# Performance work log

Hardware: AMD Instinct MI355X
Metric: run time of the kernel (lower is better)

The kernel has to match this reference:

```python
import jax, jax.numpy as jnp
import numpy as np
from jax import lax

B, C, H, W = 2, 64, 384, 384
WS = 8; NH = 4; HD = C // NH; S = WS * WS  # 64 tokens per window
EPS = 1e-5


def setup_inputs() -> dict:
    key = jax.random.key(0)
    ks = jax.random.split(key, 16)
    def n(k, shape, s=0.02):
        return jax.random.normal(k, shape, jnp.float32) * s
    return {
        "x": jax.random.normal(ks[0], (B, C, H, W), jnp.float32),
        "norm1_w": jnp.ones((C,), jnp.float32), "norm1_b": jnp.zeros((C,), jnp.float32),
        "qkv_w": n(ks[1], (3 * C, C)), "qkv_b": jnp.zeros((3 * C,), jnp.float32),
        "pos_bias": n(ks[2], (1, S, NH, NH), 0.01),  # faithful: bias over (tokens, heads, heads)
        "out_w": n(ks[3], (C, C)), "out_b": jnp.zeros((C,), jnp.float32),
        "convp_w": n(ks[4], (C, C)), "convp_b": jnp.zeros((C,), jnp.float32),
        "pw1_w": n(ks[5], (C, C, 1)), "pw1_b": jnp.zeros((C,), jnp.float32),
        "dw1_w": n(ks[6], (C, 1, 3)), "dw1_b": jnp.zeros((C,), jnp.float32),
        "tok_w": n(ks[7], (C, C)), "tok_b": jnp.zeros((C,), jnp.float32),
        "norm2_w": jnp.ones((C,), jnp.float32), "norm2_b": jnp.zeros((C,), jnp.float32),
        "leff_pw_w": n(ks[8], (C, C, 1, 1)),
        "leff_dw_w": n(ks[9], (C, 1, 3, 3)), "leff_dw_b": jnp.zeros((C,), jnp.float32),
        "fc1_w": n(ks[10], (4 * C, C)), "fc1_b": jnp.zeros((4 * C,), jnp.float32),
        "fc2_w": n(ks[11], (C, 4 * C)), "fc2_b": jnp.zeros((C,), jnp.float32),
    }


def _ln_c(x, w, b):
    # channel-wise LayerNorm (Restormer 'WithBias') on (B,C,H,W), biased variance
    mu = x.mean(axis=1, keepdims=True)
    var = ((x - mu) ** 2).mean(axis=1, keepdims=True)
    return (x - mu) / jnp.sqrt(var + EPS) * w[None, :, None, None] + b[None, :, None, None]


def _lin(x, w, b):
    return x @ w.T + b


def _win_part(x):
    # (B,C,H,W) -> (B*nw, S, C); H,W divisible by WS so pad is a no-op
    b = x.shape[0]
    x = x.reshape(b, C, H // WS, WS, W // WS, WS)
    return x.transpose(0, 2, 4, 3, 5, 1).reshape(-1, S, C)


def _win_merge(wins):
    b = wins.shape[0] // ((H // WS) * (W // WS))
    x = wins.reshape(b, H // WS, W // WS, WS, WS, C)
    return x.transpose(0, 5, 1, 3, 2, 4).reshape(b, C, H, W)


def _remsa(xw, qkv_w, qkv_b, pos_bias, out_w, out_b, convp_w, convp_b,
           pw1_w, pw1_b, dw1_w, dw1_b, tok_w, tok_b):
    bw = xw.shape[0]
    qkv = _lin(xw, qkv_w, qkv_b).reshape(bw, S, NH, 3 * HD)
    q, k, v = jnp.split(qkv, 3, axis=-1)  # each (bw, S, NH, HD)
    # Faithful to source: NO head transpose -> attention mixes across the heads axis
    scores = jnp.einsum('bshd,bsgd->bshg', q, k) * (HD ** -0.5) + pos_bias  # (bw,S,NH,NH)
    attn = jax.nn.softmax(scores, axis=-1)
    ao = jnp.einsum('bshg,bsgd->bshd', attn, v).reshape(bw, S, C)
    ao = _lin(ao, out_w, out_b)
    # convolutional branch
    xc = _lin(xw, convp_w, convp_b).transpose(0, 2, 1)  # (bw, C, S)
    xc = jnp.einsum('bcs,oc->bos', xc, pw1_w[:, :, 0]) + pw1_b[None, :, None]  # 1x1 conv1d
    xc = lax.conv_general_dilated(xc, dw1_w, (1,), 'SAME', feature_group_count=C,
                                  dimension_numbers=('NCH', 'OIH', 'NCH')) + dw1_b[None, :, None]
    xc = _lin(xc.transpose(0, 2, 1), tok_w, tok_b)
    return ao + xc


def _leff(x, pw_w, dw_w, dw_b, fc1_w, fc1_b, fc2_w, fc2_b):
    b = x.shape[0]
    y = lax.conv_general_dilated(x, pw_w, (1, 1), 'SAME',
                                 dimension_numbers=('NCHW', 'OIHW', 'NCHW'))  # 1x1, no bias
    y = lax.conv_general_dilated(y, dw_w, (1, 1), 'SAME', feature_group_count=C,
                                 dimension_numbers=('NCHW', 'OIHW', 'NCHW')) + dw_b[None, :, None, None]
    y = y.transpose(0, 2, 3, 1).reshape(b, H * W, C)
    y = jax.nn.gelu(_lin(y, fc1_w, fc1_b), approximate=False)
    y = _lin(y, fc2_w, fc2_b)
    return y.reshape(b, H, W, C).transpose(0, 3, 1, 2)


def reference(x, norm1_w, norm1_b, qkv_w, qkv_b, pos_bias, out_w, out_b,
              convp_w, convp_b, pw1_w, pw1_b, dw1_w, dw1_b, tok_w, tok_b,
              norm2_w, norm2_b, leff_pw_w, leff_dw_w, leff_dw_b,
              fc1_w, fc1_b, fc2_w, fc2_b):
    xw = _win_part(_ln_c(x, norm1_w, norm1_b))
    r = _win_merge(_remsa(xw, qkv_w, qkv_b, pos_bias, out_w, out_b, convp_w, convp_b,
                          pw1_w, pw1_b, dw1_w, dw1_b, tok_w, tok_b))
    x = x + r
    x = x + _leff(_ln_c(x, norm2_w, norm2_b), leff_pw_w, leff_dw_w, leff_dw_b,
                  fc1_w, fc1_b, fc2_w, fc2_b)
    return x
```

## Files before the change

### kernel.cpp

```cpp
#include <hip/hip_runtime.h>
#include <hip/hip_bf16.h>
#include <math.h>

#define Bn 2
#define Cc 64
#define Hh 384
#define Ww 384
#define HW (Hh*Ww)
#define Tt (Bn*HW)

using f32x4  = __attribute__((ext_vector_type(4))) float;
using bf16x8 = __attribute__((ext_vector_type(8))) short;


__device__ __forceinline__ unsigned short f2bf_u(float f) {
  return __builtin_bit_cast(unsigned short, __float2bfloat16(f));
}
__device__ __forceinline__ float bf2f(unsigned short u) {
  union { unsigned u; float f; } v; v.u = ((unsigned)u) << 16;
  return v.f;
}
__device__ __forceinline__ float gelu_exact(float v) {
  return 0.5f * v * (1.0f + erff(v * 0.70710678118654752f));
}

__device__ __forceinline__ void stage_wtile(char* dst, const float* __restrict__ g, int rs, int tid) {
#pragma unroll
  for (int half = 0; half < 2; ++half) {
    int q = tid + half * 256;
    int row = q >> 3, ks = q & 7;
    const float* gp = g + (long)row * rs + ks * 8;
    float4 a = *(const float4*)gp;
    float4 b = *(const float4*)(gp + 4);
    bf16x8 o;
    o[0] = (short)f2bf_u(a.x); o[1] = (short)f2bf_u(a.y);
    o[2] = (short)f2bf_u(a.z); o[3] = (short)f2bf_u(a.w);
    o[4] = (short)f2bf_u(b.x); o[5] = (short)f2bf_u(b.y);
    o[6] = (short)f2bf_u(b.z); o[7] = (short)f2bf_u(b.w);
    *(bf16x8*)(dst + row * 128 + ((ks * 16) ^ ((row & 7) << 4))) = o;
  }
}

__device__ __forceinline__ void mfma64(const char* sA, const char* sB, int wid, int lane, f32x4 acc[4]) {
  const int r = lane & 15, kq = lane >> 4;
#pragma unroll
  for (int kh = 0; kh < 2; ++kh) {
    const int arow = wid * 16 + r;
    bf16x8 af = *(const bf16x8*)(sA + arow * 128 + ((kh * 64 + kq * 16) ^ ((arow & 7) << 4)));
#pragma unroll
    for (int nt = 0; nt < 4; ++nt) {
      const int brow = nt * 16 + r;
      bf16x8 bfv = *(const bf16x8*)(sB + brow * 128 + ((kh * 64 + kq * 16) ^ ((brow & 7) << 4)));
      acc[nt] = __builtin_amdgcn_mfma_f32_16x16x32_bf16(af, bfv, acc[nt], 0, 0, 0);
    }
  }
}


__global__ __launch_bounds__(512, 4) void kA(
    const float* __restrict__ x, unsigned short* __restrict__ x1g, unsigned short* __restrict__ yg,
    const float* __restrict__ n1w, const float* __restrict__ n1b,
    const float* __restrict__ qkvw, const float* __restrict__ qkvb,
    const float* __restrict__ posb,
    const float* __restrict__ outw, const float* __restrict__ outb,
    const float* __restrict__ cpw, const float* __restrict__ cpb,
    const float* __restrict__ pw1w, const float* __restrict__ pw1b,
    const float* __restrict__ dw1w, const float* __restrict__ dw1b,
    const float* __restrict__ tokw, const float* __restrict__ tokb,
    const float* __restrict__ n2w, const float* __restrict__ n2b,
    const float* __restrict__ lpw) {
  __shared__ char sX[16384];
  __shared__ char sW0[8192];
  __shared__ char sW1[8192];
  __shared__ char sQ[49152];

  const int tid = threadIdx.x;
  const int lane = tid & 63, wid = tid >> 6;
  const int fr = lane & 15, kq = lane >> 4;
  const int rtok = wid * 16 + fr;
  const int c0own = kq * 16;
  const int iy = wid, ix = fr;
  const int blk = blockIdx.x;
  const int b = blk / 1152;
  const int rr = blk - b * 1152;
  const int wy = rr / 24, wxp = rr - (rr / 24) * 24;
  const int h0 = wy * 8, w0 = wxp * 16;
  const long ibase = (long)b * HW;

  float4 wr0, wr1;
  const int wrow = tid >> 3, wc0 = (tid & 7) * 8;
  auto WLOAD = [&](const float* g) {
    const float* p = g + (long)wrow * 64 + wc0;
    wr0 = *(const float4*)p; wr1 = *(const float4*)(p + 4);
  };
  auto WSTORE = [&](char* dst) {
    bf16x8 o;
    o[0]=(short)f2bf_u(wr0.x); o[1]=(short)f2bf_u(wr0.y); o[2]=(short)f2bf_u(wr0.z); o[3]=(short)f2bf_u(wr0.w);
    o[4]=(short)f2bf_u(wr1.x); o[5]=(short)f2bf_u(wr1.y); o[6]=(short)f2bf_u(wr1.z); o[7]=(short)f2bf_u(wr1.w);
    *(bf16x8*)(dst + wrow * 128 + ((2 * wc0) ^ ((wrow & 7) << 4))) = o;
  };

  WLOAD(cpw);
  const float* xb = x + ((long)(b * 64 + c0own)) * HW + (long)(h0 + iy) * Ww + (w0 + ix);
  float vx[16]; float s0 = 0.f, s1 = 0.f;
#pragma unroll
  for (int k = 0; k < 16; ++k) {
    float v = xb[(long)k * HW];
    vx[k] = v; s0 += v; s1 += v * v;
  }
  s0 += __shfl_xor(s0, 16); s0 += __shfl_xor(s0, 32);
  s1 += __shfl_xor(s1, 16); s1 += __shfl_xor(s1, 32);
  {
    float m = s0 * (1.f / 64.f);
    float ri = rsqrtf(s1 * (1.f / 64.f) - m * m + 1e-5f);
    const int swz = (rtok & 7) << 4;
#pragma unroll
    for (int q8 = 0; q8 < 2; ++q8) {
      bf16x8 o;
#pragma unroll
      for (int j = 0; j < 8; ++j) {
        int c = c0own + q8 * 8 + j;
        o[j] = (short)f2bf_u((vx[q8 * 8 + j] - m) * ri * n1w[c] + n1b[c]);
      }
      *(bf16x8*)(sX + rtok * 128 + ((c0own * 2 + q8 * 16) ^ swz)) = o;
    }
  }
  WSTORE(sW0); WLOAD(pw1w);
  __syncthreads();

  f32x4 acc[4], res[4];
  auto ZERO = [&](f32x4 a[4]) {
#pragma unroll
    for (int nt = 0; nt < 4; ++nt) a[nt] = (f32x4){0.f, 0.f, 0.f, 0.f};
  };
  auto GEMM = [&](const char* A, const char* W, f32x4 a[4]) {
#pragma unroll
    for (int kh = 0; kh < 2; ++kh) {
      const int arow = wid * 16 + fr;
      bf16x8 af = *(const bf16x8*)(A + arow * 128 + ((kh * 64 + kq * 16) ^ ((arow & 7) << 4)));
#pragma unroll
      for (int nt = 0; nt < 4; ++nt) {
        const int brow = nt * 16 + fr;
        bf16x8 bv = *(const bf16x8*)(W + brow * 128 + ((kh * 64 + kq * 16) ^ ((brow & 7) << 4)));
        a[nt] = __builtin_amdgcn_mfma_f32_16x16x32_bf16(af, bv, a[nt], 0, 0, 0);
      }
    }
  };
  auto EPI = [&](char* dst, f32x4 a[4], const float* bias) {
    const int rb = wid * 16 + kq * 4;
#pragma unroll
    for (int nt = 0; nt < 4; ++nt) {
      const int col = nt * 16 + fr;
      const float bv = bias[col];
#pragma unroll
      for (int reg = 0; reg < 4; ++reg) {
        const int row = rb + reg;
        *(unsigned short*)(dst + row * 128 + ((2 * col) ^ ((row & 7) << 4))) = f2bf_u(a[nt][reg] + bv);
      }
    }
  };
  char* t0 = sQ; char* t1 = sQ + 16384; char* t2 = sQ + 32768;
  float* sQf = (float*)sQ;

  ZERO(acc); GEMM(sX, sW0, acc); EPI(t0, acc, cpb);
  WSTORE(sW1); WLOAD(tokw);
  __syncthreads();
  ZERO(acc); GEMM(t0, sW1, acc); EPI(t1, acc, pw1b);
  WSTORE(sW0); WLOAD(qkvw);
  __syncthreads();
  {
    const int c = tid & 63, tq = tid >> 6;
    const int wl = tq >> 2, chunk = tq & 3;
    float wv0 = dw1w[c * 3], wv1 = dw1w[c * 3 + 1], wv2 = dw1w[c * 3 + 2], bia = dw1b[c];
#pragma unroll
    for (int k = 0; k < 16; ++k) {
      int s = chunk * 16 + k;
      int r0 = ((s >> 3) << 4) + wl * 8 + (s & 7);
      float v = bia + bf2f(*(const unsigned short*)(t1 + r0 * 128 + ((2 * c) ^ ((r0 & 7) << 4)))) * wv1;
      if (s > 0) {
        int rm = (((s - 1) >> 3) << 4) + wl * 8 + ((s - 1) & 7);
        v += bf2f(*(const unsigned short*)(t1 + rm * 128 + ((2 * c) ^ ((rm & 7) << 4)))) * wv0;
      }
      if (s < 63) {
        int rp = (((s + 1) >> 3) << 4) + wl * 8 + ((s + 1) & 7);
        v += bf2f(*(const unsigned short*)(t1 + rp * 128 + ((2 * c) ^ ((rp & 7) << 4)))) * wv2;
      }
      *(unsigned short*)(t0 + r0 * 128 + ((2 * c) ^ ((r0 & 7) << 4))) = f2bf_u(v);
    }
  }
  WSTORE(sW1); WLOAD(qkvw + 4096);
  __syncthreads();
  ZERO(res); GEMM(t0, sW0, res);
  __syncthreads();
  ZERO(acc); GEMM(sX, sW1, acc); EPI(t0, acc, qkvb);
  WSTORE(sW0); WLOAD(qkvw + 8192);
  __syncthreads();
  ZERO(acc); GEMM(sX, sW0, acc); EPI(t1, acc, qkvb + 64);
  WSTORE(sW1); WLOAD(outw);
  __syncthreads();
  ZERO(acc); GEMM(sX, sW1, acc); EPI(t2, acc, qkvb + 128);
  WSTORE(sW0); WLOAD(lpw);
  __syncthreads();
  {
    const int r = rtok;
    const int h = kq;
    const int s = ((r >> 4) << 3) + (r & 7);
    const int swz = (r & 7) << 4;
    auto LD16 = [&](int gcol, float* o) {
      const char* base = sQ + ((gcol >> 6) * 16384) + r * 128;
      int c0 = (gcol & 63) * 2;
      bf16x8 u = *(const bf16x8*)(base + (c0 ^ swz));
      bf16x8 w2_ = *(const bf16x8*)(base + ((c0 + 16) ^ swz));
#pragma unroll
      for (int j = 0; j < 8; ++j) {
        o[j] = bf2f((unsigned short)u[j]); o[8 + j] = bf2f((unsigned short)w2_[j]);
      }
    };
    float q0[16];
    LD16(48 * h, q0);
    float sc[4];
#pragma unroll
    for (int g = 0; g < 4; ++g) {
      float kk[16]; LD16(48 * g + 16, kk);
      float a = 0.f;
#pragma unroll
      for (int d = 0; d < 16; ++d) a += q0[d] * kk[d];
      sc[g] = a * 0.25f + posb[s * 16 + h * 4 + g];
    }
    float m = fmaxf(fmaxf(sc[0], sc[1]), fmaxf(sc[2], sc[3]));
    float e[4]; float tsum = 0.f;
#pragma unroll
    for (int g = 0; g < 4; ++g) { e[g] = __expf(sc[g] - m); tsum += e[g]; }
    float inv = 1.f / tsum;
    float ao[16];
#pragma unroll
    for (int d = 0; d < 16; ++d) ao[d] = 0.f;
#pragma unroll
    for (int g = 0; g < 4; ++g) {
      float vv[16]; LD16(48 * g + 32, vv);
#pragma unroll
      for (int d = 0; d < 16; ++d) ao[d] += e[g] * vv[d];
    }
    bf16x8 o1, o2;
#pragma unroll
    for (int j = 0; j < 8; ++j) { o1[j] = (short)f2bf_u(ao[j] * inv); o2[j] = (short)f2bf_u(ao[8 + j] * inv); }
    *(bf16x8*)(sX + r * 128 + ((h * 32) ^ swz)) = o1;
    *(bf16x8*)(sX + r * 128 + ((h * 32 + 16) ^ swz)) = o2;
  }
  WSTORE(sW1);
  __syncthreads();
  GEMM(sX, sW0, res);
  {
    const int rb = wid * 16 + kq * 4;
#pragma unroll
    for (int nt = 0; nt < 4; ++nt) {
      const int col = nt * 16 + fr;
      const float ob = outb[col] + tokb[col];
#pragma unroll
      for (int reg = 0; reg < 4; ++reg)
        sQf[(rb + reg) * 67 + col] = res[nt][reg] + ob;
    }
  }
  __syncthreads();
  {
    float ss0 = 0.f, ss1 = 0.f;
#pragma unroll
    for (int k = 0; k < 16; ++k) {
      float v = sQf[rtok * 67 + c0own + k] + vx[k];
      vx[k] = v; ss0 += v; ss1 += v * v;
    }
    ss0 += __shfl_xor(ss0, 16); ss0 += __shfl_xor(ss0, 32);
    ss1 += __shfl_xor(ss1, 16); ss1 += __shfl_xor(ss1, 32);
    float m = ss0 * (1.f / 64.f);
    float ri = rsqrtf(ss1 * (1.f / 64.f) - m * m + 1e-5f);
    const int swz = (rtok & 7) << 4;
    long t = ibase + (long)(h0 + iy) * Ww + (w0 + ix);
#pragma unroll
    for (int q8 = 0; q8 < 2; ++q8) {
      bf16x8 xo, no;
#pragma unroll
      for (int j = 0; j < 8; ++j) {
        int c = c0own + q8 * 8 + j;
        float v = vx[q8 * 8 + j];
        xo[j] = (short)f2bf_u(v);
        no[j] = (short)f2bf_u((v - m) * ri * n2w[c] + n2b[c]);
      }
      *(bf16x8*)((char*)x1g + t * 128 + (c0own + q8 * 8) * 2) = xo;
      *(bf16x8*)(sX + rtok * 128 + ((c0own * 2 + q8 * 16) ^ swz)) = no;
    }
  }
  __syncthreads();
  ZERO(acc); GEMM(sX, sW1, acc);
  {
    const int rb = wid * 16 + kq * 4;
#pragma unroll
    for (int nt = 0; nt < 4; ++nt) {
      const int col = nt * 16 + fr;
#pragma unroll
      for (int reg = 0; reg < 4; ++reg)
        sQf[(rb + reg) * 67 + col] = acc[nt][reg];
    }
  }
  __syncthreads();
  {
    long t = ibase + (long)(h0 + iy) * Ww + (w0 + ix);
#pragma unroll
    for (int q8 = 0; q8 < 2; ++q8) {
      bf16x8 o;
#pragma unroll
      for (int j = 0; j < 8; ++j)
        o[j] = (short)f2bf_u(sQf[rtok * 67 + c0own + q8 * 8 + j]);
      *(bf16x8*)((char*)yg + t * 128 + (c0own + q8 * 8) * 2) = o;
    }
  }
}


__global__ __launch_bounds__(256, 3) void kB(
    const unsigned short* __restrict__ yg, const unsigned short* __restrict__ x1g,
    float* __restrict__ out,
    const float* __restrict__ ldw, const float* __restrict__ ldb,
    const float* __restrict__ f1w, const float* __restrict__ f1b,
    const float* __restrict__ f2w, const float* __restrict__ f2b) {
  __shared__ char sZ0[8192];
  __shared__ char sZ1[8192];
  __shared__ char U[33792];
  __shared__ float wtab[640];

  const int tid = threadIdx.x;
  const int lane = tid & 63, wid = tid >> 6;
  const int bid = blockIdx.x;
  const int b = bid / 1152;
  const int r2 = bid - b * 1152;
  const int hp = r2 / 6, wseg = r2 - (r2 / 6) * 6;
  const int h0 = hp * 2, w0 = wseg * 64;
  const long ibase = (long)b * HW;
  const int cbase = lane & 15;
  const int rbase = wid * 16 + (lane >> 4) * 4;

  unsigned short x1r[2][4][4];
#pragma unroll
  for (int t = 0; t < 2; ++t) {
    const long p0t = ibase + (long)(h0 + t) * Ww + w0;
#pragma unroll
    for (int nt = 0; nt < 4; ++nt) {
      int col = nt * 16 + cbase;
#pragma unroll
      for (int reg = 0; reg < 4; ++reg)
        x1r[t][nt][reg] = x1g[(p0t + rbase + reg) * 64 + col];
    }
  }

#pragma unroll
  for (int it = 0; it < 3; ++it) {
    int idx = it * 256 + tid;
    if (idx < 576) wtab[idx] = ldw[(idx & 63) * 9 + (idx >> 6)];
    else if (idx < 640) wtab[idx] = ldb[idx - 576];
  }

  for (int it = 0; it < 9; ++it) {
    int idx = it * 256 + tid;
    if (idx >= 2112) break;
    int hr = idx / 528;
    int rq = idx - hr * 528;
    int px = rq >> 3, c8 = rq & 7;
    int h = h0 - 1 + hr, w = w0 - 1 + px;
    uint4 v = make_uint4(0, 0, 0, 0);
    if (h >= 0 && h < Hh && w >= 0 && w < Ww) {
      long t = ibase + (long)h * Ww + w;
      v = *(const uint4*)((const char*)yg + t * 128 + c8 * 16);
    }
    *(uint4*)(U + (hr * 66 + px) * 128 + c8 * 16) = v;
  }
  __syncthreads();

  {
    const int c8 = tid & 7, c0 = c8 * 8;
#pragma unroll
    for (int it = 0; it < 4; ++it) {
      int task = it * 256 + tid;
      int r = task >> 9;
      int px = (task >> 3) & 63;
      float a8[8];
#pragma unroll
      for (int j = 0; j < 8; ++j) a8[j] = wtab[576 + c0 + j];
#pragma unroll
      for (int dy = 0; dy < 3; ++dy)
#pragma unroll
        for (int dx = 0; dx < 3; ++dx) {
          bf16x8 v = *(const bf16x8*)(U + ((r + dy) * 66 + px + dx) * 128 + c8 * 16);
          const float* wk = wtab + (dy * 3 + dx) * 64 + c0;
#pragma unroll
          for (int j = 0; j < 8; ++j) a8[j] += bf2f((unsigned short)v[j]) * wk[j];
        }
      char* sZ = r ? sZ1 : sZ0;
      bf16x8 o;
#pragma unroll
      for (int j = 0; j < 8; ++j) o[j] = (short)f2bf_u(a8[j]);
      *(bf16x8*)(sZ + px * 128 + ((c8 * 16) ^ ((px & 7) << 4))) = o;
    }
  }
  __syncthreads();

  char* sW  = U;
  char* sH0 = U + 8192;
  char* sH1 = U + 16384;
  f32x4 res0[4], res1[4];
#pragma unroll
  for (int nt = 0; nt < 4; ++nt) { res0[nt] = (f32x4){0.f,0.f,0.f,0.f}; res1[nt] = (f32x4){0.f,0.f,0.f,0.f}; }

  for (int jc = 0; jc < 4; ++jc) {
    stage_wtile(sW, f1w + jc * 4096, 64, tid);
    __syncthreads();
#pragma unroll
    for (int t = 0; t < 2; ++t) {
      f32x4 acc[4];
#pragma unroll
      for (int nt = 0; nt < 4; ++nt) acc[nt] = (f32x4){0.f,0.f,0.f,0.f};
      mfma64(t ? sZ1 : sZ0, sW, wid, lane, acc);
      char* sH = t ? sH1 : sH0;
#pragma unroll
      for (int nt = 0; nt < 4; ++nt) {
        const int col = nt * 16 + cbase;
        const float bv = f1b[jc * 64 + col];
#pragma unroll
        for (int reg = 0; reg < 4; ++reg) {
          const int row = rbase + reg;
          *(unsigned short*)(sH + row * 128 + ((col * 2) ^ ((row & 7) << 4))) =
              f2bf_u(gelu_exact(acc[nt][reg] + bv));
        }
      }
    }
    __syncthreads();
    stage_wtile(sW, f2w + jc * 64, 256, tid);
    __syncthreads();
    mfma64(sH0, sW, wid, lane, res0);
    mfma64(sH1, sW, wid, lane, res1);
    __syncthreads();
  }

  float* sO = (float*)U;
#pragma unroll
  for (int t = 0; t < 2; ++t) {
    const f32x4* res = t ? res1 : res0;
#pragma unroll
    for (int nt = 0; nt < 4; ++nt) {
      const int col = nt * 16 + cbase;
      const float bv = f2b[col];
#pragma unroll
      for (int reg = 0; reg < 4; ++reg) {
        const int row = rbase + reg;
        sO[row * 65 + col] = res[nt][reg] + bv + bf2f(x1r[t][nt][reg]);
      }
    }
    __syncthreads();
#pragma unroll
    for (int it = 0; it < 16; ++it) {
      int c = it * 4 + (tid >> 6);
      int wo = tid & 63;
      out[(((long)(b * Cc + c)) * Hh + (h0 + t)) * Ww + w0 + wo] = sO[wo * 65 + c];
    }
    __syncthreads();
  }
}


extern "C" void kernel_launch(void* const* d_in, const int* in_sizes, int n_in,
                              void* d_out, int out_size, void* d_ws, size_t ws_size,
                              hipStream_t stream) {
  const float* x    = (const float*)d_in[0];
  const float* n1w  = (const float*)d_in[1];
  const float* n1b  = (const float*)d_in[2];
  const float* qkvw = (const float*)d_in[3];
  const float* qkvb = (const float*)d_in[4];
  const float* posb = (const float*)d_in[5];
  const float* outw = (const float*)d_in[6];
  const float* outb = (const float*)d_in[7];
  const float* cpw  = (const float*)d_in[8];
  const float* cpb  = (const float*)d_in[9];
  const float* pw1w = (const float*)d_in[10];
  const float* pw1b = (const float*)d_in[11];
  const float* dw1w = (const float*)d_in[12];
  const float* dw1b = (const float*)d_in[13];
  const float* tokw = (const float*)d_in[14];
  const float* tokb = (const float*)d_in[15];
  const float* n2w  = (const float*)d_in[16];
  const float* n2b  = (const float*)d_in[17];
  const float* lpw  = (const float*)d_in[18];
  const float* ldw  = (const float*)d_in[19];
  const float* ldb  = (const float*)d_in[20];
  const float* f1w  = (const float*)d_in[21];
  const float* f1b  = (const float*)d_in[22];
  const float* f2w  = (const float*)d_in[23];
  const float* f2b  = (const float*)d_in[24];
  float* out = (float*)d_out;

  unsigned short* x1 = (unsigned short*)d_ws;
  unsigned short* y  = x1 + (size_t)Tt * 64;

  kA<<<dim3(2304), dim3(512), 0, stream>>>(x, x1, y, n1w, n1b, qkvw, qkvb, posb,
                                           outw, outb, cpw, cpb, pw1w, pw1b,
                                           dw1w, dw1b, tokw, tokb, n2w, n2b, lpw);
  kB<<<dim3(2304), dim3(256), 0, stream>>>(y, x1, out, ldw, ldb, f1w, f1b, f2w, f2b);
}
```

Measured before the change: 184.7 us.

## Keep depthwise conv output in MFMA A-fragments in registers instead of LDS

The depthwise 3x3 conv in kB is remapped so each lane computes exactly the bf16 values it needs as MFMA A-operands for fc1, and keeps them in registers rather than writing them to the sZ0/sZ1 shared buffers. This removes 16KB of LDS per block and a round trip through shared memory, and launch bounds are raised from 3 to 4 blocks per CU. The staged input tile in U is XOR-swizzled to avoid bank conflicts under the new access pattern. The tighter launch bound adds register pressure, since the fragments stay live across the fc1/fc2 loop, and that may cause spills.

```diff
diff --git a/kernel.cpp b/kernel.cpp
--- a/kernel.cpp
+++ b/kernel.cpp
@@ -316,27 +316,26 @@
 }
 
 
-__global__ __launch_bounds__(256, 3) void kB(
+__global__ __launch_bounds__(256, 4) void kB(
     const unsigned short* __restrict__ yg, const unsigned short* __restrict__ x1g,
     float* __restrict__ out,
     const float* __restrict__ ldw, const float* __restrict__ ldb,
     const float* __restrict__ f1w, const float* __restrict__ f1b,
     const float* __restrict__ f2w, const float* __restrict__ f2b) {
-  __shared__ char sZ0[8192];
-  __shared__ char sZ1[8192];
   __shared__ char U[33792];
   __shared__ float wtab[640];
 
   const int tid = threadIdx.x;
   const int lane = tid & 63, wid = tid >> 6;
+  const int fr = lane & 15, kq = lane >> 4;
   const int bid = blockIdx.x;
   const int b = bid / 1152;
   const int r2 = bid - b * 1152;
   const int hp = r2 / 6, wseg = r2 - (r2 / 6) * 6;
   const int h0 = hp * 2, w0 = wseg * 64;
   const long ibase = (long)b * HW;
-  const int cbase = lane & 15;
-  const int rbase = wid * 16 + (lane >> 4) * 4;
+  const int cbase = fr;
+  const int rbase = wid * 16 + kq * 4;
 
   unsigned short x1r[2][4][4];
 #pragma unroll
@@ -370,34 +369,41 @@
       long t = ibase + (long)h * Ww + w;
       v = *(const uint4*)((const char*)yg + t * 128 + c8 * 16);
     }
-    *(uint4*)(U + (hr * 66 + px) * 128 + c8 * 16) = v;
-  }
-  __syncthreads();
-
-  {
-    const int c8 = tid & 7, c0 = c8 * 8;
-#pragma unroll
-    for (int it = 0; it < 4; ++it) {
-      int task = it * 256 + tid;
-      int r = task >> 9;
-      int px = (task >> 3) & 63;
-      float a8[8];
-#pragma unroll
-      for (int j = 0; j < 8; ++j) a8[j] = wtab[576 + c0 + j];
+    int X = hr * 66 + px;
+    *(uint4*)(U + X * 128 + ((c8 * 16) ^ ((X & 7) << 4))) = v;
+  }
+  __syncthreads();
+
+  bf16x8 afr[2][2];
+  {
+    const int pxg = wid * 16 + fr;
+#pragma unroll
+    for (int t = 0; t < 2; ++t) {
+      float z[16];
+#pragma unroll
+      for (int j = 0; j < 8; ++j) {
+        z[j] = wtab[576 + kq * 8 + j];
+        z[8 + j] = wtab[576 + 32 + kq * 8 + j];
+      }
 #pragma unroll
       for (int dy = 0; dy < 3; ++dy)
 #pragma unroll
         for (int dx = 0; dx < 3; ++dx) {
-          bf16x8 v = *(const bf16x8*)(U + ((r + dy) * 66 + px + dx) * 128 + c8 * 16);
-          const float* wk = wtab + (dy * 3 + dx) * 64 + c0;
-#pragma unroll
-          for (int j = 0; j < 8; ++j) a8[j] += bf2f((unsigned short)v[j]) * wk[j];
+          int X = (t + dy) * 66 + pxg + dx;
+          int sw = (X & 7) << 4;
+          bf16x8 u0 = *(const bf16x8*)(U + X * 128 + ((kq * 16) ^ sw));
+          bf16x8 u1 = *(const bf16x8*)(U + X * 128 + ((64 + kq * 16) ^ sw));
+          const float* wk = wtab + (dy * 3 + dx) * 64;
+#pragma unroll
+          for (int j = 0; j < 8; ++j) {
+            z[j]     += bf2f((unsigned short)u0[j]) * wk[kq * 8 + j];
+            z[8 + j] += bf2f((unsigned short)u1[j]) * wk[32 + kq * 8 + j];
+          }
         }
-      char* sZ = r ? sZ1 : sZ0;
-      bf16x8 o;
-#pragma unroll
-      for (int j = 0; j < 8; ++j) o[j] = (short)f2bf_u(a8[j]);
-      *(bf16x8*)(sZ + px * 128 + ((c8 * 16) ^ ((px & 7) << 4))) = o;
+      bf16x8 a0, a1;
+#pragma unroll
+      for (int j = 0; j < 8; ++j) { a0[j] = (short)f2bf_u(z[j]); a1[j] = (short)f2bf_u(z[8 + j]); }
+      afr[t][0] = a0; afr[t][1] = a1;
     }
   }
   __syncthreads();
@@ -417,7 +423,16 @@
       f32x4 acc[4];
 #pragma unroll
       for (int nt = 0; nt < 4; ++nt) acc[nt] = (f32x4){0.f,0.f,0.f,0.f};
-      mfma64(t ? sZ1 : sZ0, sW, wid, lane, acc);
+#pragma unroll
+      for (int kh = 0; kh < 2; ++kh) {
+        bf16x8 af = kh ? afr[t][1] : afr[t][0];
+#pragma unroll
+        for (int nt = 0; nt < 4; ++nt) {
+          const int brow = nt * 16 + fr;
+          bf16x8 bv = *(const bf16x8*)(sW + brow * 128 + ((kh * 64 + kq * 16) ^ ((brow & 7) << 4)));
+          acc[nt] = __builtin_amdgcn_mfma_f32_16x16x32_bf16(af, bv, acc[nt], 0, 0, 0);
+        }
+      }
       char* sH = t ? sH1 : sH0;
 #pragma unroll
       for (int nt = 0; nt < 4; ++nt) {
```

Measured after the change: 232.1 us. +25.7%, slower.
